# Optimization experiments

Measured on AMD Instinct MI355X. Metric: run time of the kernel, lower is better.

The kernel has to match this reference:

```python
import jax, jax.numpy as jnp
import numpy as np

NUM_HEADS = 32
MAX_BIAS_LENGTH = 1024
ROPE_BASE = 10000.0


def _rope_cos_sin(seq_len, head_dim, dtype):
    half = head_dim // 2
    inv_freq = 1.0 / (ROPE_BASE ** (jnp.arange(0, half, dtype=jnp.float32) / half))
    t = jnp.arange(seq_len, dtype=jnp.float32)
    freqs = jnp.outer(t, inv_freq)  # [S, half]
    return jnp.cos(freqs).astype(dtype), jnp.sin(freqs).astype(dtype)


def _apply_rope(x, cos, sin):
    # x: [B, S, H, D]; non-interleaved (GPT-NeoX / flash-attn style) rotary
    half = x.shape[-1] // 2
    x1, x2 = x[..., :half], x[..., half:]
    c = cos[None, :, None, :]
    s = sin[None, :, None, :]
    return jnp.concatenate([x1 * c - x2 * s, x1 * s + x2 * c], axis=-1)


def setup_inputs() -> dict:
    key = jax.random.key(0)
    ks = jax.random.split(key, 7)
    B, S, Dm = 2, 2048, 2048
    std = 1.0 / np.sqrt(Dm)
    return {
        "hidden_states": jax.random.normal(ks[0], (B, S, Dm), jnp.float32),
        "Wq": jax.random.normal(ks[1], (Dm, Dm), jnp.float32) * std,
        "Wk": jax.random.normal(ks[2], (Dm, Dm), jnp.float32) * std,
        "Wv": jax.random.normal(ks[3], (Dm, Dm), jnp.float32) * std,
        "Wo": jax.random.normal(ks[4], (Dm, Dm), jnp.float32) * std,
        "learnable_bias": jax.random.normal(ks[5], (NUM_HEADS, MAX_BIAS_LENGTH), jnp.float32) * 0.001,
        "softmax_offset": jnp.zeros((NUM_HEADS,), jnp.float32),
    }


def reference(hidden_states, Wq, Wk, Wv, Wo, learnable_bias, softmax_offset):
    B, S, Dm = hidden_states.shape
    H = NUM_HEADS
    D = Dm // H
    scale = D ** -0.5

    # projections (nn.Linear: x @ W.T)
    q = (hidden_states @ Wq.T).reshape(B, S, H, D)
    k = (hidden_states @ Wk.T).reshape(B, S, H, D)
    v = (hidden_states @ Wv.T).reshape(B, S, H, D)

    cos, sin = _rope_cos_sin(S, D, q.dtype)
    q = _apply_rope(q, cos, sin)
    k = _apply_rope(k, cos, sin)

    q = q.transpose(0, 2, 1, 3)  # [B, H, S, D]
    k = k.transpose(0, 2, 1, 3)
    v = v.transpose(0, 2, 1, 3)

    scores = jnp.einsum("bhid,bhjd->bhij", q, k) * scale  # [B, H, S, S]

    # per-diagonal learnable bias: diag = i - j in [0, MAX_BIAS_LENGTH)
    i = jnp.arange(S)[:, None]
    j = jnp.arange(S)[None, :]
    diag = i - j  # [S, S]
    causal = diag >= 0
    in_band = causal & (diag < MAX_BIAS_LENGTH)
    bias = jnp.where(in_band, learnable_bias[:, jnp.clip(diag, 0, MAX_BIAS_LENGTH - 1)], 0.0)  # [H, S, S]
    scores = scores + bias[None]
    scores = jnp.where(causal[None, None], scores, -jnp.inf)

    # softmax with learnable per-head offset (attention-sink logit)
    off = softmax_offset[None, :, None]  # [1, H, 1]
    m = jnp.maximum(jnp.max(scores, axis=-1), off)  # [B, H, S]
    p = jnp.exp(scores - m[..., None])
    denom = jnp.sum(p, axis=-1) + jnp.exp(off - m)  # [B, H, S]
    out = jnp.einsum("bhij,bhjd->bhid", p, v) / denom[..., None]

    out = out.transpose(0, 2, 1, 3).reshape(B, S, Dm)
    return out @ Wo.T
```

## Files before the change

kernel.cpp:

```cpp
#include <hip/hip_runtime.h>
#include <hip/hip_bf16.h>
#include <stdint.h>

typedef __bf16 bf16x8 __attribute__((ext_vector_type(8)));
typedef float f32x4 __attribute__((ext_vector_type(4)));
typedef unsigned short u16;
typedef u16 u16x4 __attribute__((ext_vector_type(4)));

#define S_LEN 2048
#define DMODEL 2048
#define NHEADS 32
#define BATCH 2
#define MROWS (BATCH * S_LEN)
#define BIAS_LEN 1024
#define LOG2E 1.44269504088896f

__device__ __forceinline__ u16 b16(float f) {
  union { __bf16 h; u16 u; } cv; cv.h = (__bf16)f; return cv.u;
}

__device__ __forceinline__ void gload16(const void* g, void* l) {
  __builtin_amdgcn_global_load_lds(
      (const __attribute__((address_space(1))) uint32_t*)g,
      (__attribute__((address_space(3))) uint32_t*)l, 16, 0, 0);
}

__global__ __launch_bounds__(256)
void cvt_bf16(const float* __restrict__ in, u16* __restrict__ out, int n) {
  int i = (blockIdx.x * 256 + threadIdx.x) * 4;
  if (i >= n) return;
  float4 v = *(const float4*)(in + i);
  u16x4 o = { b16(v.x), b16(v.y), b16(v.z), b16(v.w) };
  *(u16x4*)(out + i) = o;
}

__global__ __launch_bounds__(256)
void rope_tab(float* __restrict__ ct, float* __restrict__ st) {
  int idx = blockIdx.x * 256 + threadIdx.x;
  if (idx >= S_LEN * 32) return;
  int s = idx >> 5, d = idx & 31;
  float inv = exp2f((float)d * (-13.287712379549449f / 32.0f));
  float a = (float)s * inv;
  ct[idx] = cosf(a);
  st[idx] = sinf(a);
}

__global__ __launch_bounds__(256)
void bias_prep(const float* __restrict__ in, u16* __restrict__ out) {
  int i = blockIdx.x * 256 + threadIdx.x;
  out[i] = b16(in[i] * LOG2E);
}

template<int EPI>
__global__ __launch_bounds__(256)
void gemm_bt(const u16* __restrict__ A, const u16* __restrict__ Bm,
             void* __restrict__ Cout,
             const float* __restrict__ ctab, const float* __restrict__ stab)
{
  __shared__ u16 sA[128 * 64];
  __shared__ u16 sB[128 * 64];
  const int tid  = threadIdx.x;
  const int lane = tid & 63;
  const int wid  = tid >> 6;
  const int wm   = wid >> 1, wn = wid & 1;
  const int lc   = lane & 15, lr = lane >> 4;
  const int tm   = blockIdx.y * 128;
  const int tn   = blockIdx.x * 128;

  f32x4 acc[4][4] = {};

  const u16* aS[4]; const u16* bS[4];
#pragma unroll
  for (int it = 0; it < 4; ++it) {
    int u = it * 256 + tid;
    int row = u >> 3;
    int ch  = (u & 7) ^ (row & 7);
    aS[it] = A  + (size_t)(tm + row) * DMODEL + ch * 8;
    bS[it] = Bm + (size_t)(tn + row) * DMODEL + ch * 8;
  }

  for (int k0 = 0; k0 < DMODEL; k0 += 64) {
    __syncthreads();
#pragma unroll
    for (int it = 0; it < 4; ++it) {
      int u = it * 256 + tid;
      gload16(aS[it] + k0, (char*)sA + u * 16);
      gload16(bS[it] + k0, (char*)sB + u * 16);
    }
    __syncthreads();
#pragma unroll
    for (int kk = 0; kk < 2; ++kk) {
      bf16x8 af[4], bq[4];
#pragma unroll
      for (int mi = 0; mi < 4; ++mi) {
        int row = wm * 64 + mi * 16 + lc;
        int ch  = (kk * 4 + lr) ^ (row & 7);
        af[mi] = *(const bf16x8*)((const char*)sA + row * 128 + ch * 16);
      }
#pragma unroll
      for (int ni = 0; ni < 4; ++ni) {
        int row = wn * 64 + ni * 16 + lc;
        int ch  = (kk * 4 + lr) ^ (row & 7);
        bq[ni] = *(const bf16x8*)((const char*)sB + row * 128 + ch * 16);
      }
#pragma unroll
      for (int mi = 0; mi < 4; ++mi)
#pragma unroll
        for (int ni = 0; ni < 4; ++ni)
          acc[mi][ni] = __builtin_amdgcn_mfma_f32_16x16x32_bf16(af[mi], bq[ni], acc[mi][ni], 0, 0, 0);
    }
  }

  if constexpr (EPI == 4) {
    float* C = (float*)Cout;
#pragma unroll
    for (int mi = 0; mi < 4; ++mi)
#pragma unroll
      for (int ni = 0; ni < 4; ++ni)
#pragma unroll
        for (int j = 0; j < 4; ++j) {
          int r = tm + wm * 64 + mi * 16 + lr * 4 + j;
          int c = tn + wn * 64 + ni * 16 + lc;
          C[(size_t)r * DMODEL + c] = acc[mi][ni][j];
        }
  } else if constexpr (EPI == 3) {
    u16* C = (u16*)Cout;
#pragma unroll
    for (int mi = 0; mi < 4; ++mi)
#pragma unroll
      for (int ni = 0; ni < 4; ++ni) {
        int col = tn + wn * 64 + ni * 16 + lc;
        int hh = col >> 6, d = col & 63;
        int m0 = tm + wm * 64 + mi * 16 + lr * 4;
        int bb = m0 >> 11, s = m0 & 2047;
        u16x4 v = { b16(acc[mi][ni][0]), b16(acc[mi][ni][1]),
                    b16(acc[mi][ni][2]), b16(acc[mi][ni][3]) };
        *(u16x4*)(C + (((size_t)bb * NHEADS + hh) * 64 + d) * S_LEN + s) = v;
      }
  } else {
    u16* C = (u16*)Cout;
#pragma unroll
    for (int mi = 0; mi < 4; ++mi)
#pragma unroll
      for (int ni = 0; ni < 2; ++ni)
#pragma unroll
        for (int j = 0; j < 4; ++j) {
          int col = tn + wn * 64 + ni * 16 + lc;
          int hh = col >> 6, dl = col & 63;
          int r = tm + wm * 64 + mi * 16 + lr * 4 + j;
          int bb = r >> 11, s = r & 2047;
          float x1 = acc[mi][ni][j], x2 = acc[mi][ni + 2][j];
          float cv = ctab[s * 32 + dl], sv = stab[s * 32 + dl];
          float o1 = x1 * cv - x2 * sv;
          float o2 = x1 * sv + x2 * cv;
          if constexpr (EPI == 1) {
            o1 *= 0.125f * LOG2E; o2 *= 0.125f * LOG2E;
          }
          size_t base = (((size_t)bb * NHEADS + hh) * S_LEN + s) * 64 + dl;
          C[base]      = b16(o1);
          C[base + 32] = b16(o2);
        }
  }
}

__global__ __launch_bounds__(512, 6)
void attn_kernel(const u16* __restrict__ Q, const u16* __restrict__ K,
                 const u16* __restrict__ V, const u16* __restrict__ bias16,
                 const float* __restrict__ offg, u16* __restrict__ O)
{
  __shared__ __align__(16) u16 sK[2][64 * 64];
  __shared__ __align__(16) u16 sV[2][64 * 64];
  __shared__ __align__(16) u16 sP[8][16 * 40];
  __shared__ __align__(8)  u16 sBiasT[1152];

  const int tid = threadIdx.x, lane = tid & 63, wid = tid >> 6;
  const int lc = lane & 15, lr = lane >> 4;
  const int L  = blockIdx.x;
  const int p  = 15 - (L >> 6);
  const int bh = L & 63;
  const int h  = bh & 31;
  const int b  = bh >> 5;
  const int qw = p * 128 + wid * 16;
  const int nt = 2 * p + 2;

  for (int i = tid; i < 1152; i += 512) {
    int dd = i - 64;
    sBiasT[i] = (dd >= 0 && dd < BIAS_LEN) ? bias16[h * BIAS_LEN + dd] : (u16)0;
  }
  const float off = offg[h] * LOG2E;

  const u16* qp = Q + ((size_t)bh * S_LEN + qw + lc) * 64;
  bf16x8 aq0 = *(const bf16x8*)(qp + lr * 8);
  bf16x8 aq1 = *(const bf16x8*)(qp + 32 + lr * 8);

  const int srow = tid >> 3;
  const int sch  = (tid & 7) ^ (srow & 7);
  const u16* kSrc = K + ((size_t)bh * S_LEN + srow) * 64 + sch * 8;
  const u16* vSrc = V + ((size_t)bh * 64 + srow) * S_LEN + sch * 8;

  int offK[4][2], offV[2][4];
#pragma unroll
  for (int f = 0; f < 4; ++f) {
    int row = f * 16 + lc;
    offK[f][0] = row * 128 + ((lr) ^ (row & 7)) * 16;
    offK[f][1] = row * 128 + ((4 + lr) ^ (row & 7)) * 16;
  }
#pragma unroll
  for (int kk = 0; kk < 2; ++kk)
#pragma unroll
    for (int f2 = 0; f2 < 4; ++f2) {
      int drow = f2 * 16 + lc;
      offV[kk][f2] = drow * 128 + ((kk * 4 + lr) ^ (drow & 7)) * 16;
    }

  float lsum = exp2f(off);
  f32x4 o[4] = {};

  gload16(kSrc, (char*)sK[0] + tid * 16);
  gload16(vSrc, (char*)sV[0] + tid * 16);
  __syncthreads();

  for (int t = 0; t < nt; ++t) {
    const int cur = t & 1;
    if (t + 1 < nt) {
      gload16(kSrc + (size_t)(t + 1) * 4096, (char*)sK[cur ^ 1] + tid * 16);
      gload16(vSrc + (t + 1) * 64,           (char*)sV[cur ^ 1] + tid * 16);
    }

    const int dqt = qw - t * 64;
    if (dqt >= 0) {
      f32x4 sc[4];
      __builtin_amdgcn_s_setprio(1);
#pragma unroll
      for (int f = 0; f < 4; ++f) {
        bf16x8 k0 = *(const bf16x8*)((const char*)sK[cur] + offK[f][0]);
        bf16x8 k1 = *(const bf16x8*)((const char*)sK[cur] + offK[f][1]);
        f32x4 z = {};
        z     = __builtin_amdgcn_mfma_f32_16x16x32_bf16(k0, aq0, z, 0, 0, 0);
        sc[f] = __builtin_amdgcn_mfma_f32_16x16x32_bf16(k1, aq1, z, 0, 0, 0);
      }
      __builtin_amdgcn_s_setprio(0);

      const int db = dqt + lc;
      float pvv[4][4];
      if (dqt < 1088) {
        const int ib = db + 64 - lr * 4;
#pragma unroll
        for (int f = 0; f < 4; ++f)
#pragma unroll
          for (int j = 0; j < 4; ++j) {
            float bb = __uint_as_float((uint32_t)sBiasT[ib - f * 16 - j] << 16);
            pvv[f][j] = sc[f][j] + bb;
          }
        if (dqt < 64) {
#pragma unroll
          for (int f = 0; f < 4; ++f)
#pragma unroll
            for (int j = 0; j < 4; ++j) {
              int dd = db - (f * 16 + lr * 4 + j);
              pvv[f][j] = (dd >= 0) ? pvv[f][j] : -1e30f;
            }
        }
      } else {
#pragma unroll
        for (int f = 0; f < 4; ++f)
#pragma unroll
          for (int j = 0; j < 4; ++j)
            pvv[f][j] = sc[f][j];
      }

      float rsum = 0.0f;
#pragma unroll
      for (int f = 0; f < 4; ++f)
#pragma unroll
        for (int j = 0; j < 4; ++j) {
          float pe = exp2f(pvv[f][j]);
          pvv[f][j] = pe;
          rsum += pe;
        }
      rsum += __shfl_xor(rsum, 16, 64);
      rsum += __shfl_xor(rsum, 32, 64);
      lsum += rsum;

      u16* myP = sP[wid];
#pragma unroll
      for (int kk = 0; kk < 2; ++kk) {
#pragma unroll
        for (int fl = 0; fl < 2; ++fl) {
          int f = kk * 2 + fl;
          u16x4 w = { b16(pvv[f][0]), b16(pvv[f][1]), b16(pvv[f][2]), b16(pvv[f][3]) };
          *(u16x4*)(myP + lc * 40 + fl * 16 + lr * 4) = w;
        }
        asm volatile("s_waitcnt lgkmcnt(0)" ::: "memory");
        __builtin_amdgcn_sched_barrier(0);
        bf16x8 ap = *(const bf16x8*)(myP + lc * 40 + lr * 8);
        __builtin_amdgcn_s_setprio(1);
#pragma unroll
        for (int f2 = 0; f2 < 4; ++f2) {
          bf16x8 bv = *(const bf16x8*)((const char*)sV[cur] + offV[kk][f2]);
          o[f2] = __builtin_amdgcn_mfma_f32_16x16x32_bf16(ap, bv, o[f2], 0, 0, 0);
        }
        __builtin_amdgcn_s_setprio(0);
      }
    }
    __syncthreads();
  }

  float ls[4];
#pragma unroll
  for (int j = 0; j < 4; ++j) ls[j] = 1.0f / __shfl(lsum, lr * 4 + j, 64);
#pragma unroll
  for (int f2 = 0; f2 < 4; ++f2)
#pragma unroll
    for (int j = 0; j < 4; ++j) {
      int i = qw + lr * 4 + j;
      int d = f2 * 16 + lc;
      size_t addr = (((size_t)(b * S_LEN + i)) * NHEADS + h) * 64 + d;
      O[addr] = b16(o[f2][j] * ls[j]);
    }
}

extern "C" void kernel_launch(void* const* d_in, const int* in_sizes, int n_in,
                              void* d_out, int out_size, void* d_ws, size_t ws_size,
                              hipStream_t stream)
{
  const float* hs   = (const float*)d_in[0];
  const float* Wq   = (const float*)d_in[1];
  const float* Wk   = (const float*)d_in[2];
  const float* Wv   = (const float*)d_in[3];
  const float* Wo   = (const float*)d_in[4];
  const float* bias = (const float*)d_in[5];
  const float* off  = (const float*)d_in[6];

  char* p = (char*)d_ws;
  u16* hs_b = (u16*)p; p += (size_t)MROWS * DMODEL * 2;
  u16* wq_b = (u16*)p; p += (size_t)DMODEL * DMODEL * 2;
  u16* wk_b = (u16*)p; p += (size_t)DMODEL * DMODEL * 2;
  u16* wv_b = (u16*)p; p += (size_t)DMODEL * DMODEL * 2;
  u16* wo_b = (u16*)p; p += (size_t)DMODEL * DMODEL * 2;
  u16* qf   = (u16*)p; p += (size_t)MROWS * DMODEL * 2;
  u16* kf   = (u16*)p; p += (size_t)MROWS * DMODEL * 2;
  u16* vt   = (u16*)p; p += (size_t)MROWS * DMODEL * 2;
  u16* att  = (u16*)p; p += (size_t)MROWS * DMODEL * 2;
  float* ct = (float*)p; p += (size_t)S_LEN * 32 * 4;
  float* st = (float*)p; p += (size_t)S_LEN * 32 * 4;
  u16* b16t = (u16*)p; p += (size_t)NHEADS * BIAS_LEN * 2;
  (void)ws_size; (void)in_sizes; (void)n_in; (void)out_size;

  cvt_bf16<<<(MROWS * DMODEL) / 1024, 256, 0, stream>>>(hs, hs_b, MROWS * DMODEL);
  cvt_bf16<<<(DMODEL * DMODEL) / 1024, 256, 0, stream>>>(Wq, wq_b, DMODEL * DMODEL);
  cvt_bf16<<<(DMODEL * DMODEL) / 1024, 256, 0, stream>>>(Wk, wk_b, DMODEL * DMODEL);
  cvt_bf16<<<(DMODEL * DMODEL) / 1024, 256, 0, stream>>>(Wv, wv_b, DMODEL * DMODEL);
  cvt_bf16<<<(DMODEL * DMODEL) / 1024, 256, 0, stream>>>(Wo, wo_b, DMODEL * DMODEL);
  rope_tab<<<(S_LEN * 32) / 256, 256, 0, stream>>>(ct, st);
  bias_prep<<<(NHEADS * BIAS_LEN) / 256, 256, 0, stream>>>(bias, b16t);

  dim3 g(DMODEL / 128, MROWS / 128);
  gemm_bt<1><<<g, 256, 0, stream>>>(hs_b, wq_b, qf, ct, st);
  gemm_bt<2><<<g, 256, 0, stream>>>(hs_b, wk_b, kf, ct, st);
  gemm_bt<3><<<g, 256, 0, stream>>>(hs_b, wv_b, vt, nullptr, nullptr);
  attn_kernel<<<dim3(16 * 64), 512, 0, stream>>>(qf, kf, vt, b16t, off, att);
  gemm_bt<4><<<g, 256, 0, stream>>>(att, wo_b, d_out, nullptr, nullptr);
}
```

Baseline: 311.0 us.

## Batch weight conversion and QKV GEMMs, fold bias into MFMA accumulator init

```diff
diff --git a/kernel.cpp b/kernel.cpp
--- a/kernel.cpp
+++ b/kernel.cpp
@@ -32,6 +32,18 @@
   float4 v = *(const float4*)(in + i);
   u16x4 o = { b16(v.x), b16(v.y), b16(v.z), b16(v.w) };
   *(u16x4*)(out + i) = o;
+}
+
+__global__ __launch_bounds__(256)
+void cvt_w4(const float* __restrict__ w0, const float* __restrict__ w1,
+            const float* __restrict__ w2, const float* __restrict__ w3,
+            u16* __restrict__ out) {
+  const float* src = (blockIdx.y == 0) ? w0 : (blockIdx.y == 1) ? w1
+                   : (blockIdx.y == 2) ? w2 : w3;
+  int i = (blockIdx.x * 256 + threadIdx.x) * 4;
+  float4 v = *(const float4*)(src + i);
+  u16x4 o = { b16(v.x), b16(v.y), b16(v.z), b16(v.w) };
+  *(u16x4*)(out + (size_t)blockIdx.y * DMODEL * DMODEL + i) = o;
 }
 
 __global__ __launch_bounds__(256)
@@ -51,11 +63,55 @@
   out[i] = b16(in[i] * LOG2E);
 }
 
-template<int EPI>
-__global__ __launch_bounds__(256)
-void gemm_bt(const u16* __restrict__ A, const u16* __restrict__ Bm,
-             void* __restrict__ Cout,
-             const float* __restrict__ ctab, const float* __restrict__ stab)
+#define GEMM_MAIN_LOOP(Aptr, Bptr)                                            \
+  f32x4 acc[4][4] = {};                                                       \
+  const u16* aS[4]; const u16* bS[4];                                         \
+  _Pragma("unroll")                                                           \
+  for (int it = 0; it < 4; ++it) {                                            \
+    int u = it * 256 + tid;                                                   \
+    int row = u >> 3;                                                         \
+    int ch  = (u & 7) ^ (row & 7);                                            \
+    aS[it] = (Aptr) + (size_t)(tm + row) * DMODEL + ch * 8;                   \
+    bS[it] = (Bptr) + (size_t)(tn + row) * DMODEL + ch * 8;                   \
+  }                                                                           \
+  for (int k0 = 0; k0 < DMODEL; k0 += 64) {                                   \
+    __syncthreads();                                                          \
+    _Pragma("unroll")                                                         \
+    for (int it = 0; it < 4; ++it) {                                          \
+      int u = it * 256 + tid;                                                 \
+      gload16(aS[it] + k0, (char*)sA + u * 16);                               \
+      gload16(bS[it] + k0, (char*)sB + u * 16);                               \
+    }                                                                         \
+    __syncthreads();                                                          \
+    _Pragma("unroll")                                                         \
+    for (int kk = 0; kk < 2; ++kk) {                                          \
+      bf16x8 af[4], bq[4];                                                    \
+      _Pragma("unroll")                                                       \
+      for (int mi = 0; mi < 4; ++mi) {                                        \
+        int row = wm * 64 + mi * 16 + lc;                                     \
+        int ch  = (kk * 4 + lr) ^ (row & 7);                                  \
+        af[mi] = *(const bf16x8*)((const char*)sA + row * 128 + ch * 16);     \
+      }                                                                       \
+      _Pragma("unroll")                                                       \
+      for (int ni = 0; ni < 4; ++ni) {                                        \
+        int row = wn * 64 + ni * 16 + lc;                                     \
+        int ch  = (kk * 4 + lr) ^ (row & 7);                                  \
+        bq[ni] = *(const bf16x8*)((const char*)sB + row * 128 + ch * 16);     \
+      }                                                                       \
+      _Pragma("unroll")                                                       \
+      for (int mi = 0; mi < 4; ++mi)                                          \
+        _Pragma("unroll")                                                     \
+        for (int ni = 0; ni < 4; ++ni)                                        \
+          acc[mi][ni] = __builtin_amdgcn_mfma_f32_16x16x32_bf16(              \
+              af[mi], bq[ni], acc[mi][ni], 0, 0, 0);                          \
+    }                                                                         \
+  }
+
+__global__ __launch_bounds__(256)
+void gemm_qkv(const u16* __restrict__ A, const u16* __restrict__ Wqb,
+              const u16* __restrict__ Wkb, const u16* __restrict__ Wvb,
+              u16* __restrict__ qf, u16* __restrict__ kf, u16* __restrict__ vt,
+              const float* __restrict__ ctab, const float* __restrict__ stab)
 {
   __shared__ u16 sA[128 * 64];
   __shared__ u16 sB[128 * 64];
@@ -64,67 +120,15 @@
   const int wid  = tid >> 6;
   const int wm   = wid >> 1, wn = wid & 1;
   const int lc   = lane & 15, lr = lane >> 4;
+  const int which = blockIdx.x >> 4;
+  const int tn   = (blockIdx.x & 15) * 128;
   const int tm   = blockIdx.y * 128;
-  const int tn   = blockIdx.x * 128;
-
-  f32x4 acc[4][4] = {};
-
-  const u16* aS[4]; const u16* bS[4];
-#pragma unroll
-  for (int it = 0; it < 4; ++it) {
-    int u = it * 256 + tid;
-    int row = u >> 3;
-    int ch  = (u & 7) ^ (row & 7);
-    aS[it] = A  + (size_t)(tm + row) * DMODEL + ch * 8;
-    bS[it] = Bm + (size_t)(tn + row) * DMODEL + ch * 8;
-  }
-
-  for (int k0 = 0; k0 < DMODEL; k0 += 64) {
-    __syncthreads();
-#pragma unroll
-    for (int it = 0; it < 4; ++it) {
-      int u = it * 256 + tid;
-      gload16(aS[it] + k0, (char*)sA + u * 16);
-      gload16(bS[it] + k0, (char*)sB + u * 16);
-    }
-    __syncthreads();
-#pragma unroll
-    for (int kk = 0; kk < 2; ++kk) {
-      bf16x8 af[4], bq[4];
-#pragma unroll
-      for (int mi = 0; mi < 4; ++mi) {
-        int row = wm * 64 + mi * 16 + lc;
-        int ch  = (kk * 4 + lr) ^ (row & 7);
-        af[mi] = *(const bf16x8*)((const char*)sA + row * 128 + ch * 16);
-      }
-#pragma unroll
-      for (int ni = 0; ni < 4; ++ni) {
-        int row = wn * 64 + ni * 16 + lc;
-        int ch  = (kk * 4 + lr) ^ (row & 7);
-        bq[ni] = *(const bf16x8*)((const char*)sB + row * 128 + ch * 16);
-      }
-#pragma unroll
-      for (int mi = 0; mi < 4; ++mi)
-#pragma unroll
-        for (int ni = 0; ni < 4; ++ni)
-          acc[mi][ni] = __builtin_amdgcn_mfma_f32_16x16x32_bf16(af[mi], bq[ni], acc[mi][ni], 0, 0, 0);
-    }
-  }
-
-  if constexpr (EPI == 4) {
-    float* C = (float*)Cout;
-#pragma unroll
-    for (int mi = 0; mi < 4; ++mi)
-#pragma unroll
-      for (int ni = 0; ni < 4; ++ni)
-#pragma unroll
-        for (int j = 0; j < 4; ++j) {
-          int r = tm + wm * 64 + mi * 16 + lr * 4 + j;
-          int c = tn + wn * 64 + ni * 16 + lc;
-          C[(size_t)r * DMODEL + c] = acc[mi][ni][j];
-        }
-  } else if constexpr (EPI == 3) {
-    u16* C = (u16*)Cout;
+  const u16* Bm = (which == 0) ? Wqb : (which == 1) ? Wkb : Wvb;
+
+  GEMM_MAIN_LOOP(A, Bm)
+
+  if (which == 2) {
+    u16* C = vt;
 #pragma unroll
     for (int mi = 0; mi < 4; ++mi)
 #pragma unroll
@@ -138,7 +142,8 @@
         *(u16x4*)(C + (((size_t)bb * NHEADS + hh) * 64 + d) * S_LEN + s) = v;
       }
   } else {
-    u16* C = (u16*)Cout;
+    u16* C = (which == 0) ? qf : kf;
+    const float scl = (which == 0) ? 0.125f * LOG2E : 1.0f;
 #pragma unroll
     for (int mi = 0; mi < 4; ++mi)
 #pragma unroll
@@ -151,16 +156,41 @@
           int bb = r >> 11, s = r & 2047;
           float x1 = acc[mi][ni][j], x2 = acc[mi][ni + 2][j];
           float cv = ctab[s * 32 + dl], sv = stab[s * 32 + dl];
-          float o1 = x1 * cv - x2 * sv;
-          float o2 = x1 * sv + x2 * cv;
-          if constexpr (EPI == 1) {
-            o1 *= 0.125f * LOG2E; o2 *= 0.125f * LOG2E;
-          }
+          float o1 = (x1 * cv - x2 * sv) * scl;
+          float o2 = (x1 * sv + x2 * cv) * scl;
           size_t base = (((size_t)bb * NHEADS + hh) * S_LEN + s) * 64 + dl;
           C[base]      = b16(o1);
           C[base + 32] = b16(o2);
         }
   }
+}
+
+__global__ __launch_bounds__(256)
+void gemm_out(const u16* __restrict__ A, const u16* __restrict__ Bm,
+              float* __restrict__ C)
+{
+  __shared__ u16 sA[128 * 64];
+  __shared__ u16 sB[128 * 64];
+  const int tid  = threadIdx.x;
+  const int lane = tid & 63;
+  const int wid  = tid >> 6;
+  const int wm   = wid >> 1, wn = wid & 1;
+  const int lc   = lane & 15, lr = lane >> 4;
+  const int tn   = blockIdx.x * 128;
+  const int tm   = blockIdx.y * 128;
+
+  GEMM_MAIN_LOOP(A, Bm)
+
+#pragma unroll
+  for (int mi = 0; mi < 4; ++mi)
+#pragma unroll
+    for (int ni = 0; ni < 4; ++ni)
+#pragma unroll
+      for (int j = 0; j < 4; ++j) {
+        int r = tm + wm * 64 + mi * 16 + lr * 4 + j;
+        int c = tn + wn * 64 + ni * 16 + lc;
+        C[(size_t)r * DMODEL + c] = acc[mi][ni][j];
+      }
 }
 
 __global__ __launch_bounds__(512, 6)
@@ -170,7 +200,7 @@
 {
   __shared__ __align__(16) u16 sK[2][64 * 64];
   __shared__ __align__(16) u16 sV[2][64 * 64];
-  __shared__ __align__(16) u16 sP[8][16 * 40];
+  __shared__ __align__(16) u16 sP[8][16 * 72];
   __shared__ __align__(8)  u16 sBiasT[1152];
 
   const int tid = threadIdx.x, lane = tid & 63, wid = tid >> 6;
@@ -213,7 +243,7 @@
       offV[kk][f2] = drow * 128 + ((kk * 4 + lr) ^ (drow & 7)) * 16;
     }
 
-  float lsum = exp2f(off);
+  float lsum = 0.0f;
   f32x4 o[4] = {};
 
   gload16(kSrc, (char*)sK[0] + tid * 16);
@@ -229,83 +259,81 @@
 
     const int dqt = qw - t * 64;
     if (dqt >= 0) {
+      const int db = dqt + lc;
+      const bool inband = (dqt < 1088);
       f32x4 sc[4];
       __builtin_amdgcn_s_setprio(1);
 #pragma unroll
       for (int f = 0; f < 4; ++f) {
+        f32x4 z;
+        if (inband) {
+          const int ib = db + 64 - lr * 4 - f * 16;
+#pragma unroll
+          for (int j = 0; j < 4; ++j)
+            z[j] = __uint_as_float((uint32_t)sBiasT[ib - j] << 16);
+        } else {
+          z[0] = z[1] = z[2] = z[3] = 0.0f;
+        }
         bf16x8 k0 = *(const bf16x8*)((const char*)sK[cur] + offK[f][0]);
         bf16x8 k1 = *(const bf16x8*)((const char*)sK[cur] + offK[f][1]);
-        f32x4 z = {};
         z     = __builtin_amdgcn_mfma_f32_16x16x32_bf16(k0, aq0, z, 0, 0, 0);
         sc[f] = __builtin_amdgcn_mfma_f32_16x16x32_bf16(k1, aq1, z, 0, 0, 0);
       }
       __builtin_amdgcn_s_setprio(0);
 
-      const int db = dqt + lc;
       float pvv[4][4];
-      if (dqt < 1088) {
-        const int ib = db + 64 - lr * 4;
+      if (dqt < 64) {
 #pragma unroll
         for (int f = 0; f < 4; ++f)
 #pragma unroll
           for (int j = 0; j < 4; ++j) {
-            float bb = __uint_as_float((uint32_t)sBiasT[ib - f * 16 - j] << 16);
-            pvv[f][j] = sc[f][j] + bb;
+            int dd = db - (f * 16 + lr * 4 + j);
+            pvv[f][j] = (dd >= 0) ? sc[f][j] : -1e30f;
           }
-        if (dqt < 64) {
-#pragma unroll
-          for (int f = 0; f < 4; ++f)
-#pragma unroll
-            for (int j = 0; j < 4; ++j) {
-              int dd = db - (f * 16 + lr * 4 + j);
-              pvv[f][j] = (dd >= 0) ? pvv[f][j] : -1e30f;
-            }
-        }
       } else {
 #pragma unroll
         for (int f = 0; f < 4; ++f)
 #pragma unroll
-          for (int j = 0; j < 4; ++j)
-            pvv[f][j] = sc[f][j];
-      }
-
-      float rsum = 0.0f;
+          for (int j = 0; j < 4; ++j) pvv[f][j] = sc[f][j];
+      }
 #pragma unroll
       for (int f = 0; f < 4; ++f)
 #pragma unroll
         for (int j = 0; j < 4; ++j) {
           float pe = exp2f(pvv[f][j]);
           pvv[f][j] = pe;
-          rsum += pe;
+          lsum += pe;
         }
-      rsum += __shfl_xor(rsum, 16, 64);
-      rsum += __shfl_xor(rsum, 32, 64);
-      lsum += rsum;
 
       u16* myP = sP[wid];
 #pragma unroll
-      for (int kk = 0; kk < 2; ++kk) {
-#pragma unroll
-        for (int fl = 0; fl < 2; ++fl) {
-          int f = kk * 2 + fl;
-          u16x4 w = { b16(pvv[f][0]), b16(pvv[f][1]), b16(pvv[f][2]), b16(pvv[f][3]) };
-          *(u16x4*)(myP + lc * 40 + fl * 16 + lr * 4) = w;
-        }
-        asm volatile("s_waitcnt lgkmcnt(0)" ::: "memory");
-        __builtin_amdgcn_sched_barrier(0);
-        bf16x8 ap = *(const bf16x8*)(myP + lc * 40 + lr * 8);
-        __builtin_amdgcn_s_setprio(1);
-#pragma unroll
-        for (int f2 = 0; f2 < 4; ++f2) {
-          bf16x8 bv = *(const bf16x8*)((const char*)sV[cur] + offV[kk][f2]);
-          o[f2] = __builtin_amdgcn_mfma_f32_16x16x32_bf16(ap, bv, o[f2], 0, 0, 0);
-        }
-        __builtin_amdgcn_s_setprio(0);
-      }
+      for (int f = 0; f < 4; ++f) {
+        u16x4 w = { b16(pvv[f][0]), b16(pvv[f][1]), b16(pvv[f][2]), b16(pvv[f][3]) };
+        *(u16x4*)(myP + lc * 72 + f * 16 + lr * 4) = w;
+      }
+      asm volatile("s_waitcnt lgkmcnt(0)" ::: "memory");
+      __builtin_amdgcn_sched_barrier(0);
+      bf16x8 ap0 = *(const bf16x8*)(myP + lc * 72 + lr * 8);
+      bf16x8 ap1 = *(const bf16x8*)(myP + lc * 72 + 32 + lr * 8);
+      __builtin_amdgcn_s_setprio(1);
+#pragma unroll
+      for (int f2 = 0; f2 < 4; ++f2) {
+        bf16x8 bv = *(const bf16x8*)((const char*)sV[cur] + offV[0][f2]);
+        o[f2] = __builtin_amdgcn_mfma_f32_16x16x32_bf16(ap0, bv, o[f2], 0, 0, 0);
+      }
+#pragma unroll
+      for (int f2 = 0; f2 < 4; ++f2) {
+        bf16x8 bv = *(const bf16x8*)((const char*)sV[cur] + offV[1][f2]);
+        o[f2] = __builtin_amdgcn_mfma_f32_16x16x32_bf16(ap1, bv, o[f2], 0, 0, 0);
+      }
+      __builtin_amdgcn_s_setprio(0);
     }
     __syncthreads();
   }
 
+  lsum += __shfl_xor(lsum, 16, 64);
+  lsum += __shfl_xor(lsum, 32, 64);
+  lsum += exp2f(off);
   float ls[4];
 #pragma unroll
   for (int j = 0; j < 4; ++j) ls[j] = 1.0f / __shfl(lsum, lr * 4 + j, 64);
@@ -348,17 +376,12 @@
   (void)ws_size; (void)in_sizes; (void)n_in; (void)out_size;
 
   cvt_bf16<<<(MROWS * DMODEL) / 1024, 256, 0, stream>>>(hs, hs_b, MROWS * DMODEL);
-  cvt_bf16<<<(DMODEL * DMODEL) / 1024, 256, 0, stream>>>(Wq, wq_b, DMODEL * DMODEL);
-  cvt_bf16<<<(DMODEL * DMODEL) / 1024, 256, 0, stream>>>(Wk, wk_b, DMODEL * DMODEL);
-  cvt_bf16<<<(DMODEL * DMODEL) / 1024, 256, 0, stream>>>(Wv, wv_b, DMODEL * DMODEL);
-  cvt_bf16<<<(DMODEL * DMODEL) / 1024, 256, 0, stream>>>(Wo, wo_b, DMODEL * DMODEL);
+  cvt_w4<<<dim3((DMODEL * DMODEL) / 1024, 4), 256, 0, stream>>>(Wq, Wk, Wv, Wo, wq_b);
   rope_tab<<<(S_LEN * 32) / 256, 256, 0, stream>>>(ct, st);
   bias_prep<<<(NHEADS * BIAS_LEN) / 256, 256, 0, stream>>>(bias, b16t);
 
-  dim3 g(DMODEL / 128, MROWS / 128);
-  gemm_bt<1><<<g, 256, 0, stream>>>(hs_b, wq_b, qf, ct, st);
-  gemm_bt<2><<<g, 256, 0, stream>>>(hs_b, wk_b, kf, ct, st);
-  gemm_bt<3><<<g, 256, 0, stream>>>(hs_b, wv_b, vt, nullptr, nullptr);
+  gemm_qkv<<<dim3(48, MROWS / 128), 256, 0, stream>>>(hs_b, wq_b, wk_b, wv_b,
+                                                      qf, kf, vt, ct, st);
   attn_kernel<<<dim3(16 * 64), 512, 0, stream>>>(qf, kf, vt, b16t, off, att);
-  gemm_bt<4><<<g, 256, 0, stream>>>(att, wo_b, d_out, nullptr, nullptr);
-}
+  gemm_out<<<dim3(DMODEL / 128, MROWS / 128), 256, 0, stream>>>(att, wo_b, (float*)d_out);
+}
```

Result: faster. 286.7 us (-7.8%).

## Fuse QKV projections into pipelined 256x256 GEMM and streamline attention inner loop

Applied to the files above, without the earlier changes.

```diff
diff --git a/kernel.cpp b/kernel.cpp
--- a/kernel.cpp
+++ b/kernel.cpp
@@ -32,6 +32,18 @@
   float4 v = *(const float4*)(in + i);
   u16x4 o = { b16(v.x), b16(v.y), b16(v.z), b16(v.w) };
   *(u16x4*)(out + i) = o;
+}
+
+__global__ __launch_bounds__(256)
+void cvt_w4(const float* __restrict__ w0, const float* __restrict__ w1,
+            const float* __restrict__ w2, const float* __restrict__ w3,
+            u16* __restrict__ out) {
+  const float* src = (blockIdx.y == 0) ? w0 : (blockIdx.y == 1) ? w1
+                   : (blockIdx.y == 2) ? w2 : w3;
+  int i = (blockIdx.x * 256 + threadIdx.x) * 4;
+  float4 v = *(const float4*)(src + i);
+  u16x4 o = { b16(v.x), b16(v.y), b16(v.z), b16(v.w) };
+  *(u16x4*)(out + (size_t)blockIdx.y * DMODEL * DMODEL + i) = o;
 }
 
 __global__ __launch_bounds__(256)
@@ -51,24 +63,153 @@
   out[i] = b16(in[i] * LOG2E);
 }
 
-template<int EPI>
+#define NT 32
+
+#define STG_A(buf, h, t) { \
+    gload16(aS0 + (size_t)(h) * 128 * DMODEL + (t) * 64, (char*)sA[buf][h] + tid * 16); \
+    gload16(aS0 + (size_t)((h) * 128 + 64) * DMODEL + (t) * 64, (char*)sA[buf][h] + (512 + tid) * 16); }
+#define STG_B(buf, h, t) { \
+    gload16(bS0 + (size_t)(h) * 128 * DMODEL + (t) * 64, (char*)sB[buf][h] + tid * 16); \
+    gload16(bS0 + (size_t)((h) * 128 + 64) * DMODEL + (t) * 64, (char*)sB[buf][h] + (512 + tid) * 16); }
+#define LOAD_B(b, kk) { _Pragma("unroll") \
+    for (int ni = 0; ni < 4; ++ni) \
+      bq[ni] = *(const bf16x8*)((const char*)sB[b][wn >> 1] + offB[ni][kk]); }
+#define LOAD_A(b, q, kk) { _Pragma("unroll") \
+    for (int mi = 0; mi < 4; ++mi) \
+      af[mi] = *(const bf16x8*)((const char*)sA[b][wm] + offA[q][mi][kk]); }
+#define MFMA16(q) { __builtin_amdgcn_s_setprio(1); \
+    _Pragma("unroll") for (int mi = 0; mi < 4; ++mi) \
+      _Pragma("unroll") for (int ni = 0; ni < 4; ++ni) \
+        acc[(q) * 4 + mi][ni] = __builtin_amdgcn_mfma_f32_16x16x32_bf16( \
+            af[mi], bq[ni], acc[(q) * 4 + mi][ni], 0, 0, 0); \
+    __builtin_amdgcn_s_setprio(0); }
+#define LGKM { asm volatile("s_waitcnt lgkmcnt(0)" ::: "memory"); \
+               __builtin_amdgcn_sched_barrier(0); }
+#define BARR { __builtin_amdgcn_s_barrier(); __builtin_amdgcn_sched_barrier(0); }
+#define VM2 { asm volatile("s_waitcnt vmcnt(2)" ::: "memory"); \
+              __builtin_amdgcn_sched_barrier(0); }
+#define VM0 { asm volatile("s_waitcnt vmcnt(0)" ::: "memory"); \
+              __builtin_amdgcn_sched_barrier(0); }
+
+__global__ __launch_bounds__(512, 2)
+void gemm_qkv8(const u16* __restrict__ A, const u16* __restrict__ W,
+               u16* __restrict__ qf, u16* __restrict__ kf, u16* __restrict__ vt,
+               const float* __restrict__ ctab, const float* __restrict__ stab)
+{
+  __shared__ u16 sA[2][2][128 * 64];
+  __shared__ u16 sB[2][2][128 * 64];
+  const int tid = threadIdx.x, lane = tid & 63, wid = tid >> 6;
+  const int wm = wid >> 2, wn = wid & 3;
+  const int lc = lane & 15, lr = lane >> 4;
+  const int L = blockIdx.x;
+  const int which = L >> 7;
+  const int rr = L & 127;
+  const int tmi = rr >> 3, tni = rr & 7;
+  const size_t tm = (size_t)tmi * 256, tn = (size_t)tni * 256;
+  const u16* Bm = W + (size_t)which * DMODEL * DMODEL;
+
+  const int r0 = tid >> 3, c0 = (tid & 7) ^ (r0 & 7);
+  const u16* aS0 = A  + (tm + r0) * DMODEL + c0 * 8;
+  const u16* bS0 = Bm + (tn + r0) * DMODEL + c0 * 8;
+
+  int offA[2][4][2], offB[4][2];
+#pragma unroll
+  for (int q = 0; q < 2; ++q)
+#pragma unroll
+    for (int mi = 0; mi < 4; ++mi) {
+      int row = q * 64 + mi * 16 + lc;
+#pragma unroll
+      for (int kk = 0; kk < 2; ++kk)
+        offA[q][mi][kk] = row * 128 + ((kk * 4 + lr) ^ (row & 7)) * 16;
+    }
+#pragma unroll
+  for (int ni = 0; ni < 4; ++ni) {
+    int row = (wn & 1) * 64 + ni * 16 + lc;
+#pragma unroll
+    for (int kk = 0; kk < 2; ++kk)
+      offB[ni][kk] = row * 128 + ((kk * 4 + lr) ^ (row & 7)) * 16;
+  }
+
+  f32x4 acc[8][4] = {};
+  bf16x8 af[4], bq[4];
+
+  STG_B(0, 0, 0); STG_B(0, 1, 0); STG_A(0, 0, 0); STG_A(0, 1, 0); STG_B(1, 0, 1);
+  VM2; BARR;
+
+  for (int i = 0; i < NT / 2; ++i) {
+    const int t1 = 2 * i + 1, t2 = 2 * i + 2, t3 = 2 * i + 3;
+    LOAD_B(0, 0); LOAD_A(0, 0, 0); STG_B(1, 1, t1); LGKM; MFMA16(0);
+    LOAD_A(0, 1, 0); STG_A(1, 0, t1); LGKM; MFMA16(1);
+    LOAD_B(0, 1); LOAD_A(0, 0, 1); STG_A(1, 1, t1); LGKM; MFMA16(0);
+    BARR;
+    LOAD_A(0, 1, 1); if (t2 < NT) STG_B(0, 0, t2); LGKM; MFMA16(1);
+    if (t2 < NT) { VM2; } else { VM0; }
+    BARR;
+    LOAD_B(1, 0); LOAD_A(1, 0, 0); if (t2 < NT) STG_B(0, 1, t2); LGKM; MFMA16(0);
+    LOAD_A(1, 1, 0); if (t2 < NT) STG_A(0, 0, t2); LGKM; MFMA16(1);
+    LOAD_B(1, 1); LOAD_A(1, 0, 1); if (t2 < NT) STG_A(0, 1, t2); LGKM; MFMA16(0);
+    BARR;
+    LOAD_A(1, 1, 1); if (t3 < NT) STG_B(1, 0, t3); LGKM; MFMA16(1);
+    if (t3 < NT) { VM2; } else { VM0; }
+    BARR;
+  }
+
+  if (which == 2) {
+#pragma unroll
+    for (int q = 0; q < 2; ++q)
+#pragma unroll
+      for (int mi = 0; mi < 4; ++mi)
+#pragma unroll
+        for (int ni = 0; ni < 4; ++ni) {
+          int col = (int)tn + wn * 64 + ni * 16 + lc;
+          int hh = col >> 6, d = col & 63;
+          int m0 = (int)tm + wm * 128 + q * 64 + mi * 16 + lr * 4;
+          int bb = m0 >> 11, s = m0 & 2047;
+          f32x4 a = acc[q * 4 + mi][ni];
+          u16x4 v = { b16(a[0]), b16(a[1]), b16(a[2]), b16(a[3]) };
+          *(u16x4*)(vt + (((size_t)bb * NHEADS + hh) * 64 + d) * S_LEN + s) = v;
+        }
+  } else {
+    u16* C = (which == 0) ? qf : kf;
+    const float scl = (which == 0) ? 0.125f * LOG2E : 1.0f;
+#pragma unroll
+    for (int q = 0; q < 2; ++q)
+#pragma unroll
+      for (int mi = 0; mi < 4; ++mi)
+#pragma unroll
+        for (int ni = 0; ni < 2; ++ni)
+#pragma unroll
+          for (int j = 0; j < 4; ++j) {
+            int col = (int)tn + wn * 64 + ni * 16 + lc;
+            int hh = col >> 6, dl = col & 63;
+            int r = (int)tm + wm * 128 + q * 64 + mi * 16 + lr * 4 + j;
+            int bb = r >> 11, s = r & 2047;
+            float x1 = acc[q * 4 + mi][ni][j], x2 = acc[q * 4 + mi][ni + 2][j];
+            float cv = ctab[s * 32 + dl], sv = stab[s * 32 + dl];
+            float o1 = (x1 * cv - x2 * sv) * scl;
+            float o2 = (x1 * sv + x2 * cv) * scl;
+            size_t base = (((size_t)bb * NHEADS + hh) * S_LEN + s) * 64 + dl;
+            C[base]      = b16(o1);
+            C[base + 32] = b16(o2);
+          }
+  }
+}
+
 __global__ __launch_bounds__(256)
-void gemm_bt(const u16* __restrict__ A, const u16* __restrict__ Bm,
-             void* __restrict__ Cout,
-             const float* __restrict__ ctab, const float* __restrict__ stab)
+void gemm_out(const u16* __restrict__ A, const u16* __restrict__ Bm,
+              float* __restrict__ C)
 {
-  __shared__ u16 sA[128 * 64];
-  __shared__ u16 sB[128 * 64];
+  __shared__ u16 sOA[128 * 64];
+  __shared__ u16 sOB[128 * 64];
   const int tid  = threadIdx.x;
   const int lane = tid & 63;
   const int wid  = tid >> 6;
   const int wm   = wid >> 1, wn = wid & 1;
   const int lc   = lane & 15, lr = lane >> 4;
+  const int tn   = blockIdx.x * 128;
   const int tm   = blockIdx.y * 128;
-  const int tn   = blockIdx.x * 128;
 
   f32x4 acc[4][4] = {};
-
   const u16* aS[4]; const u16* bS[4];
 #pragma unroll
   for (int it = 0; it < 4; ++it) {
@@ -78,89 +219,47 @@
     aS[it] = A  + (size_t)(tm + row) * DMODEL + ch * 8;
     bS[it] = Bm + (size_t)(tn + row) * DMODEL + ch * 8;
   }
-
   for (int k0 = 0; k0 < DMODEL; k0 += 64) {
     __syncthreads();
 #pragma unroll
     for (int it = 0; it < 4; ++it) {
       int u = it * 256 + tid;
-      gload16(aS[it] + k0, (char*)sA + u * 16);
-      gload16(bS[it] + k0, (char*)sB + u * 16);
+      gload16(aS[it] + k0, (char*)sOA + u * 16);
+      gload16(bS[it] + k0, (char*)sOB + u * 16);
     }
     __syncthreads();
 #pragma unroll
     for (int kk = 0; kk < 2; ++kk) {
-      bf16x8 af[4], bq[4];
+      bf16x8 af[4], bqv[4];
 #pragma unroll
       for (int mi = 0; mi < 4; ++mi) {
         int row = wm * 64 + mi * 16 + lc;
         int ch  = (kk * 4 + lr) ^ (row & 7);
-        af[mi] = *(const bf16x8*)((const char*)sA + row * 128 + ch * 16);
+        af[mi] = *(const bf16x8*)((const char*)sOA + row * 128 + ch * 16);
       }
 #pragma unroll
       for (int ni = 0; ni < 4; ++ni) {
         int row = wn * 64 + ni * 16 + lc;
         int ch  = (kk * 4 + lr) ^ (row & 7);
-        bq[ni] = *(const bf16x8*)((const char*)sB + row * 128 + ch * 16);
+        bqv[ni] = *(const bf16x8*)((const char*)sOB + row * 128 + ch * 16);
       }
 #pragma unroll
       for (int mi = 0; mi < 4; ++mi)
 #pragma unroll
         for (int ni = 0; ni < 4; ++ni)
-          acc[mi][ni] = __builtin_amdgcn_mfma_f32_16x16x32_bf16(af[mi], bq[ni], acc[mi][ni], 0, 0, 0);
-    }
-  }
-
-  if constexpr (EPI == 4) {
-    float* C = (float*)Cout;
-#pragma unroll
-    for (int mi = 0; mi < 4; ++mi)
-#pragma unroll
-      for (int ni = 0; ni < 4; ++ni)
-#pragma unroll
-        for (int j = 0; j < 4; ++j) {
-          int r = tm + wm * 64 + mi * 16 + lr * 4 + j;
-          int c = tn + wn * 64 + ni * 16 + lc;
-          C[(size_t)r * DMODEL + c] = acc[mi][ni][j];
-        }
-  } else if constexpr (EPI == 3) {
-    u16* C = (u16*)Cout;
-#pragma unroll
-    for (int mi = 0; mi < 4; ++mi)
-#pragma unroll
-      for (int ni = 0; ni < 4; ++ni) {
-        int col = tn + wn * 64 + ni * 16 + lc;
-        int hh = col >> 6, d = col & 63;
-        int m0 = tm + wm * 64 + mi * 16 + lr * 4;
-        int bb = m0 >> 11, s = m0 & 2047;
-        u16x4 v = { b16(acc[mi][ni][0]), b16(acc[mi][ni][1]),
-                    b16(acc[mi][ni][2]), b16(acc[mi][ni][3]) };
-        *(u16x4*)(C + (((size_t)bb * NHEADS + hh) * 64 + d) * S_LEN + s) = v;
-      }
-  } else {
-    u16* C = (u16*)Cout;
-#pragma unroll
-    for (int mi = 0; mi < 4; ++mi)
-#pragma unroll
-      for (int ni = 0; ni < 2; ++ni)
-#pragma unroll
-        for (int j = 0; j < 4; ++j) {
-          int col = tn + wn * 64 + ni * 16 + lc;
-          int hh = col >> 6, dl = col & 63;
-          int r = tm + wm * 64 + mi * 16 + lr * 4 + j;
-          int bb = r >> 11, s = r & 2047;
-          float x1 = acc[mi][ni][j], x2 = acc[mi][ni + 2][j];
-          float cv = ctab[s * 32 + dl], sv = stab[s * 32 + dl];
-          float o1 = x1 * cv - x2 * sv;
-          float o2 = x1 * sv + x2 * cv;
-          if constexpr (EPI == 1) {
-            o1 *= 0.125f * LOG2E; o2 *= 0.125f * LOG2E;
-          }
-          size_t base = (((size_t)bb * NHEADS + hh) * S_LEN + s) * 64 + dl;
-          C[base]      = b16(o1);
-          C[base + 32] = b16(o2);
-        }
-  }
+          acc[mi][ni] = __builtin_amdgcn_mfma_f32_16x16x32_bf16(af[mi], bqv[ni], acc[mi][ni], 0, 0, 0);
+    }
+  }
+#pragma unroll
+  for (int mi = 0; mi < 4; ++mi)
+#pragma unroll
+    for (int ni = 0; ni < 4; ++ni)
+#pragma unroll
+      for (int j = 0; j < 4; ++j) {
+        int r = tm + wm * 64 + mi * 16 + lr * 4 + j;
+        int c = tn + wn * 64 + ni * 16 + lc;
+        C[(size_t)r * DMODEL + c] = acc[mi][ni][j];
+      }
 }
 
 __global__ __launch_bounds__(512, 6)
@@ -170,7 +269,7 @@
 {
   __shared__ __align__(16) u16 sK[2][64 * 64];
   __shared__ __align__(16) u16 sV[2][64 * 64];
-  __shared__ __align__(16) u16 sP[8][16 * 40];
+  __shared__ __align__(16) u16 sP[8][16 * 72];
   __shared__ __align__(8)  u16 sBiasT[1152];
 
   const int tid = threadIdx.x, lane = tid & 63, wid = tid >> 6;
@@ -213,7 +312,7 @@
       offV[kk][f2] = drow * 128 + ((kk * 4 + lr) ^ (drow & 7)) * 16;
     }
 
-  float lsum = exp2f(off);
+  float lsum = 0.0f;
   f32x4 o[4] = {};
 
   gload16(kSrc, (char*)sK[0] + tid * 16);
@@ -229,83 +328,81 @@
 
     const int dqt = qw - t * 64;
     if (dqt >= 0) {
+      const int db = dqt + lc;
+      const bool inband = (dqt < 1088);
       f32x4 sc[4];
       __builtin_amdgcn_s_setprio(1);
 #pragma unroll
       for (int f = 0; f < 4; ++f) {
+        f32x4 z;
+        if (inband) {
+          const int ib = db + 64 - lr * 4 - f * 16;
+#pragma unroll
+          for (int j = 0; j < 4; ++j)
+            z[j] = __uint_as_float((uint32_t)sBiasT[ib - j] << 16);
+        } else {
+          z[0] = z[1] = z[2] = z[3] = 0.0f;
+        }
         bf16x8 k0 = *(const bf16x8*)((const char*)sK[cur] + offK[f][0]);
         bf16x8 k1 = *(const bf16x8*)((const char*)sK[cur] + offK[f][1]);
-        f32x4 z = {};
         z     = __builtin_amdgcn_mfma_f32_16x16x32_bf16(k0, aq0, z, 0, 0, 0);
         sc[f] = __builtin_amdgcn_mfma_f32_16x16x32_bf16(k1, aq1, z, 0, 0, 0);
       }
       __builtin_amdgcn_s_setprio(0);
 
-      const int db = dqt + lc;
       float pvv[4][4];
-      if (dqt < 1088) {
-        const int ib = db + 64 - lr * 4;
+      if (dqt < 64) {
 #pragma unroll
         for (int f = 0; f < 4; ++f)
 #pragma unroll
           for (int j = 0; j < 4; ++j) {
-            float bb = __uint_as_float((uint32_t)sBiasT[ib - f * 16 - j] << 16);
-            pvv[f][j] = sc[f][j] + bb;
+            int dd = db - (f * 16 + lr * 4 + j);
+            pvv[f][j] = (dd >= 0) ? sc[f][j] : -1e30f;
           }
-        if (dqt < 64) {
-#pragma unroll
-          for (int f = 0; f < 4; ++f)
-#pragma unroll
-            for (int j = 0; j < 4; ++j) {
-              int dd = db - (f * 16 + lr * 4 + j);
-              pvv[f][j] = (dd >= 0) ? pvv[f][j] : -1e30f;
-            }
-        }
       } else {
 #pragma unroll
         for (int f = 0; f < 4; ++f)
 #pragma unroll
-          for (int j = 0; j < 4; ++j)
-            pvv[f][j] = sc[f][j];
-      }
-
-      float rsum = 0.0f;
+          for (int j = 0; j < 4; ++j) pvv[f][j] = sc[f][j];
+      }
 #pragma unroll
       for (int f = 0; f < 4; ++f)
 #pragma unroll
         for (int j = 0; j < 4; ++j) {
           float pe = exp2f(pvv[f][j]);
           pvv[f][j] = pe;
-          rsum += pe;
+          lsum += pe;
         }
-      rsum += __shfl_xor(rsum, 16, 64);
-      rsum += __shfl_xor(rsum, 32, 64);
-      lsum += rsum;
 
       u16* myP = sP[wid];
 #pragma unroll
-      for (int kk = 0; kk < 2; ++kk) {
-#pragma unroll
-        for (int fl = 0; fl < 2; ++fl) {
-          int f = kk * 2 + fl;
-          u16x4 w = { b16(pvv[f][0]), b16(pvv[f][1]), b16(pvv[f][2]), b16(pvv[f][3]) };
-          *(u16x4*)(myP + lc * 40 + fl * 16 + lr * 4) = w;
-        }
-        asm volatile("s_waitcnt lgkmcnt(0)" ::: "memory");
-        __builtin_amdgcn_sched_barrier(0);
-        bf16x8 ap = *(const bf16x8*)(myP + lc * 40 + lr * 8);
-        __builtin_amdgcn_s_setprio(1);
-#pragma unroll
-        for (int f2 = 0; f2 < 4; ++f2) {
-          bf16x8 bv = *(const bf16x8*)((const char*)sV[cur] + offV[kk][f2]);
-          o[f2] = __builtin_amdgcn_mfma_f32_16x16x32_bf16(ap, bv, o[f2], 0, 0, 0);
-        }
-        __builtin_amdgcn_s_setprio(0);
-      }
+      for (int f = 0; f < 4; ++f) {
+        u16x4 w = { b16(pvv[f][0]), b16(pvv[f][1]), b16(pvv[f][2]), b16(pvv[f][3]) };
+        *(u16x4*)(myP + lc * 72 + f * 16 + lr * 4) = w;
+      }
+      asm volatile("s_waitcnt lgkmcnt(0)" ::: "memory");
+      __builtin_amdgcn_sched_barrier(0);
+      bf16x8 ap0 = *(const bf16x8*)(myP + lc * 72 + lr * 8);
+      bf16x8 ap1 = *(const bf16x8*)(myP + lc * 72 + 32 + lr * 8);
+      __builtin_amdgcn_s_setprio(1);
+#pragma unroll
+      for (int f2 = 0; f2 < 4; ++f2) {
+        bf16x8 bv = *(const bf16x8*)((const char*)sV[cur] + offV[0][f2]);
+        o[f2] = __builtin_amdgcn_mfma_f32_16x16x32_bf16(ap0, bv, o[f2], 0, 0, 0);
+      }
+#pragma unroll
+      for (int f2 = 0; f2 < 4; ++f2) {
+        bf16x8 bv = *(const bf16x8*)((const char*)sV[cur] + offV[1][f2]);
+        o[f2] = __builtin_amdgcn_mfma_f32_16x16x32_bf16(ap1, bv, o[f2], 0, 0, 0);
+      }
+      __builtin_amdgcn_s_setprio(0);
     }
     __syncthreads();
   }
 
+  lsum += __shfl_xor(lsum, 16, 64);
+  lsum += __shfl_xor(lsum, 32, 64);
+  lsum += exp2f(off);
   float ls[4];
 #pragma unroll
   for (int j = 0; j < 4; ++j) ls[j] = 1.0f / __shfl(lsum, lr * 4 + j, 64);
@@ -348,17 +445,11 @@
   (void)ws_size; (void)in_sizes; (void)n_in; (void)out_size;
 
   cvt_bf16<<<(MROWS * DMODEL) / 1024, 256, 0, stream>>>(hs, hs_b, MROWS * DMODEL);
-  cvt_bf16<<<(DMODEL * DMODEL) / 1024, 256, 0, stream>>>(Wq, wq_b, DMODEL * DMODEL);
-  cvt_bf16<<<(DMODEL * DMODEL) / 1024, 256, 0, stream>>>(Wk, wk_b, DMODEL * DMODEL);
-  cvt_bf16<<<(DMODEL * DMODEL) / 1024, 256, 0, stream>>>(Wv, wv_b, DMODEL * DMODEL);
-  cvt_bf16<<<(DMODEL * DMODEL) / 1024, 256, 0, stream>>>(Wo, wo_b, DMODEL * DMODEL);
+  cvt_w4<<<dim3((DMODEL * DMODEL) / 1024, 4), 256, 0, stream>>>(Wq, Wk, Wv, Wo, wq_b);
   rope_tab<<<(S_LEN * 32) / 256, 256, 0, stream>>>(ct, st);
   bias_prep<<<(NHEADS * BIAS_LEN) / 256, 256, 0, stream>>>(bias, b16t);
 
-  dim3 g(DMODEL / 128, MROWS / 128);
-  gemm_bt<1><<<g, 256, 0, stream>>>(hs_b, wq_b, qf, ct, st);
-  gemm_bt<2><<<g, 256, 0, stream>>>(hs_b, wk_b, kf, ct, st);
-  gemm_bt<3><<<g, 256, 0, stream>>>(hs_b, wv_b, vt, nullptr, nullptr);
+  gemm_qkv8<<<dim3(3 * 128), 512, 0, stream>>>(hs_b, wq_b, qf, kf, vt, ct, st);
   attn_kernel<<<dim3(16 * 64), 512, 0, stream>>>(qf, kf, vt, b16t, off, att);
-  gemm_bt<4><<<g, 256, 0, stream>>>(att, wo_b, d_out, nullptr, nullptr);
-}
+  gemm_out<<<dim3(DMODEL / 128, MROWS / 128), 256, 0, stream>>>(att, wo_b, (float*)d_out);
+}
```

Result: faster. 291.8 us (-6.2%).
